# Kernel tuning notes

Hardware: AMD Instinct MI355X
Metric: run time of the kernel (lower is better)

Reference implementation:

```python
import jax, jax.numpy as jnp
import numpy as np

N_NODES = 50000
N_EDGES = 200000
IN_DIM = 16
NODE_DIM = 64
EDGE_DIM = 16
HIDDEN = 256
NUM_LAYERS = 4  # 1 NNConv + 3 GINConv


def setup_inputs() -> dict:
    key = jax.random.key(0)
    ks = jax.random.split(key, 20)
    s = 0.05
    inp = {
        "x": jax.random.normal(ks[0], (N_NODES, IN_DIM), dtype=jnp.float32),
        "edge_index": jax.random.randint(ks[1], (2, N_EDGES), 0, N_NODES, dtype=jnp.int64),
        "edge_attr": jax.random.normal(ks[2], (N_EDGES, EDGE_DIM), dtype=jnp.float32),
        # edge-NN (per-edge weight generator): attr_dim -> 256 -> 1024 -> in*out, ELU after each
        "enn_w1": jax.random.normal(ks[3], (EDGE_DIM, 256), dtype=jnp.float32) * s,
        "enn_b1": jnp.zeros((256,), dtype=jnp.float32),
        "enn_w2": jax.random.normal(ks[4], (256, 1024), dtype=jnp.float32) * s,
        "enn_b2": jnp.zeros((1024,), dtype=jnp.float32),
        "enn_w3": jax.random.normal(ks[5], (1024, IN_DIM * NODE_DIM), dtype=jnp.float32) * s,
        "enn_b3": jnp.zeros((IN_DIM * NODE_DIM,), dtype=jnp.float32),
        # NNConv root weight + bias
        "root_w": jax.random.normal(ks[6], (IN_DIM, NODE_DIM), dtype=jnp.float32) * s,
        "root_b": jnp.zeros((NODE_DIM,), dtype=jnp.float32),
        # 3 GIN MLPs (stacked): node_dim -> hidden -> hidden -> node_dim
        "gin_w1": jax.random.normal(ks[7], (3, NODE_DIM, HIDDEN), dtype=jnp.float32) * s,
        "gin_b1": jnp.zeros((3, HIDDEN), dtype=jnp.float32),
        "gin_w2": jax.random.normal(ks[8], (3, HIDDEN, HIDDEN), dtype=jnp.float32) * s,
        "gin_b2": jnp.zeros((3, HIDDEN), dtype=jnp.float32),
        "gin_w3": jax.random.normal(ks[9], (3, HIDDEN, NODE_DIM), dtype=jnp.float32) * s,
        "gin_b3": jnp.zeros((3, NODE_DIM), dtype=jnp.float32),
    }
    return inp


def _elu(x):
    return jax.nn.elu(x)


def reference(x, edge_index, edge_attr,
              enn_w1, enn_b1, enn_w2, enn_b2, enn_w3, enn_b3,
              root_w, root_b,
              gin_w1, gin_b1, gin_w2, gin_b2, gin_w3, gin_b3):
    src = edge_index[0]  # x_j (message source)
    dst = edge_index[1]  # i (aggregation target)

    # ---- Layer 0: NNConv with per-edge MLP-generated weights ----
    h = _elu(edge_attr @ enn_w1 + enn_b1)
    h = _elu(h @ enn_w2 + enn_b2)
    w_e = _elu(h @ enn_w3 + enn_b3).reshape(-1, IN_DIM, NODE_DIM)  # [E, in, out]
    msg = jnp.einsum('ei,eio->eo', x[src], w_e)                    # [E, node_dim]
    agg = jax.ops.segment_sum(msg, dst, num_segments=N_NODES)     # scatter-add
    x_cur = x @ root_w + agg + root_b                              # [N, node_dim]
    node_emb = [x_cur]

    # ---- Layers 1..3: GINConv (eps=0) with 3-layer MLP ----
    for l in range(NUM_LAYERS - 1):
        x_in = _elu(x_cur)
        nbr = jax.ops.segment_sum(x_in[src], dst, num_segments=N_NODES)
        h = x_in + nbr  # (1 + eps) * x + sum_j x_j, eps = 0
        h = _elu(h @ gin_w1[l] + gin_b1[l])
        h = _elu(h @ gin_w2[l] + gin_b2[l])
        x_cur = h @ gin_w3[l] + gin_b3[l]
        node_emb.append(x_cur)

    return jnp.stack(node_emb, axis=2)  # [N, node_dim, num_layers]
```

## Files before the change

kernel.cpp:

```cpp
#include <hip/hip_runtime.h>
#include <hip/hip_bf16.h>


#define NN 50000
#define EE 200000

typedef unsigned short u16;
typedef __attribute__((ext_vector_type(8))) short frag8;
typedef __attribute__((ext_vector_type(4))) float f32x4;

__device__ __forceinline__ float bf2f(u16 u) {
    union { unsigned int i; float f; } v; v.i = ((unsigned int)u) << 16; return v.f;
}
__device__ __forceinline__ u16 f2bf(float f) {
    union { float f; unsigned int i; } v; v.f = f;
    return (u16)((v.i + 0x7fffu + ((v.i >> 16) & 1u)) >> 16);
}
__device__ __forceinline__ float eluf(float v) {
    return v > 0.f ? v : __expf(v) - 1.f;
}

__global__ void probe_f32(const u16* __restrict__ raw, int* __restrict__ cnt) {
    int t = threadIdx.x;
    int c = 0;
    for (int j = t; j < 1024; j += 256) {
        unsigned e = (raw[j] >> 7) & 0xFF;
        if (e >= 0xBF) c++;
    }
    if (c) atomicAdd(cnt, c);
}
__global__ void cvt_bf16(const void* __restrict__ src, u16* __restrict__ dst, long n,
                         const int* __restrict__ cnt) {
    long i = (long)blockIdx.x * 256 + threadIdx.x;
    if (i >= n) return;
    if (*cnt >= 8) dst[i] = f2bf(((const float*)src)[i]);
    else           dst[i] = ((const u16*)src)[i];
}

__global__ void detect_idx64(const unsigned long long* __restrict__ p, int* __restrict__ flag) {
    long t = (long)blockIdx.x * 256 + threadIdx.x;
    if (t < EE) {
        unsigned long long v = p[t];
        if (v >> 31) atomicOr(flag, 1);
    }
}
__global__ void convert_idx(const void* __restrict__ raw, const int* __restrict__ flag,
                            int* __restrict__ s_out, int* __restrict__ d_out) {
    long t = (long)blockIdx.x * 256 + threadIdx.x;
    if (t >= EE) return;
    if (*flag) {
        const int* q = (const int*)raw;
        s_out[t] = q[t];
        d_out[t] = q[EE + t];
    } else {
        const long long* q = (const long long*)raw;
        s_out[t] = (int)q[t];
        d_out[t] = (int)q[EE + t];
    }
}

__global__ void transpose_bf16(const u16* __restrict__ in, u16* __restrict__ out, int K, int N) {
    long idx = (long)blockIdx.x * 256 + threadIdx.x;
    if (idx < (long)K * N) {
        int k = (int)(idx / N);
        int n = (int)(idx % N);
        out[(long)n * K + k] = in[idx];
    }
}

__global__ void edge_mlp1(const u16* __restrict__ attr, const u16* __restrict__ w1,
                          const u16* __restrict__ b1, u16* __restrict__ h1, int ce) {
    __shared__ u16 sa[256];
    const int t = threadIdx.x;
    const int e0 = blockIdx.x * 16;
    const int cnt = min(16, ce - e0);
    sa[t] = (t < cnt * 16) ? attr[(long)e0 * 16 + t] : (u16)0;
    float w[16];
    #pragma unroll
    for (int i = 0; i < 16; ++i) w[i] = bf2f(w1[i * 256 + t]);
    const float bb = bf2f(b1[t]);
    __syncthreads();
    for (int e = 0; e < cnt; ++e) {
        float v = bb;
        #pragma unroll
        for (int i = 0; i < 16; ++i) v += bf2f(sa[e * 16 + i]) * w[i];
        h1[(long)(e0 + e) * 256 + t] = f2bf(eluf(v));
    }
}

__device__ __forceinline__ void stage_tile(const u16* g, long row_base, long max_row,
                                           int kstride, int k0, u16* s, int t) {
    int wave = t >> 6;
    #pragma unroll
    for (int j = 0; j < 2; ++j) {
        int c = t + 256 * j;
        long r = row_base + (c >> 2);
        if (r > max_row) r = max_row;
        const u16* gp = g + r * (long)kstride + k0 + (c & 3) * 8;
        __builtin_amdgcn_global_load_lds(
            (__attribute__((address_space(1))) void*)(void*)gp,
            (__attribute__((address_space(3))) void*)((char*)s + wave * 1024 + j * 4096),
            16, 0, 0);
    }
}

__global__ __launch_bounds__(256)
void gemm_bt_bias_elu(const u16* __restrict__ A, const u16* __restrict__ BT,
                      const u16* __restrict__ bias, u16* __restrict__ C,
                      int M, int K, int N, int mpx, int lognt) {
    const int bid = blockIdx.x;
    const int xcd = bid & 7;
    const int j = bid >> 3;
    const int m_idx = xcd * mpx + (j >> lognt);
    const int n_idx = j & ((1 << lognt) - 1);
    const int num_m = (M + 127) >> 7;
    if (m_idx >= num_m) return;

    __shared__ __align__(16) u16 sA[128 * 32];
    __shared__ __align__(16) u16 sB[128 * 32];
    const int t = threadIdx.x;
    const int lane = t & 63;
    const int wave = t >> 6;
    const int wr = wave >> 1, wc = wave & 1;
    const int quad = lane >> 4, l16 = lane & 15;
    const long m0 = (long)m_idx * 128;
    const int n0 = n_idx * 128;

    f32x4 acc[4][4];
    const f32x4 z4 = {0.f, 0.f, 0.f, 0.f};
    #pragma unroll
    for (int mi = 0; mi < 4; ++mi)
        #pragma unroll
        for (int ni = 0; ni < 4; ++ni)
            acc[mi][ni] = z4;

    for (int k0 = 0; k0 < K; k0 += 32) {
        stage_tile(A, m0, (long)M - 1, K, k0, sA, t);
        stage_tile(BT, n0, (long)N - 1, K, k0, sB, t);
        __syncthreads();
        frag8 af[4], bfv[4];
        #pragma unroll
        for (int mi = 0; mi < 4; ++mi)
            af[mi] = *(const frag8*)(sA + (wr * 64 + mi * 16 + l16) * 32 + quad * 8);
        #pragma unroll
        for (int ni = 0; ni < 4; ++ni)
            bfv[ni] = *(const frag8*)(sB + (wc * 64 + ni * 16 + l16) * 32 + quad * 8);
        #pragma unroll
        for (int mi = 0; mi < 4; ++mi)
            #pragma unroll
            for (int ni = 0; ni < 4; ++ni)
                acc[mi][ni] = __builtin_amdgcn_mfma_f32_16x16x32_bf16(af[mi], bfv[ni], acc[mi][ni], 0, 0, 0);
        __syncthreads();
    }

    #pragma unroll
    for (int mi = 0; mi < 4; ++mi) {
        #pragma unroll
        for (int r = 0; r < 4; ++r) {
            long row = m0 + wr * 64 + mi * 16 + quad * 4 + r;
            if (row < M) {
                #pragma unroll
                for (int ni = 0; ni < 4; ++ni) {
                    int col = n0 + wc * 64 + ni * 16 + l16;
                    float v = acc[mi][ni][r] + bf2f(bias[col]);
                    C[row * (long)N + col] = f2bf(eluf(v));
                }
            }
        }
    }
}


#define QPHASE(PA0, PA1, PB0, PB1, QM, QN, LDA, LDB, VMW, STREG, SG, SRB, SRM, SCL, SKT) \
  do {                                                                           \
    if (LDA) {                                                                   \
      _Pragma("unroll")                                                          \
      for (int mi = 0; mi < 4; ++mi) {                                           \
        av[mi][0] = *(const frag8*)((PA0) + ((QM) * 4 + mi) * 2048);             \
        av[mi][1] = *(const frag8*)((PA1) + ((QM) * 4 + mi) * 2048);             \
      }                                                                          \
    }                                                                            \
    if ((LDB) >= 0) {                                                            \
      _Pragma("unroll")                                                          \
      for (int ni = 0; ni < 2; ++ni) {                                           \
        bv[(LDB) & 1][ni][0] = *(const frag8*)((PB0) + (((LDB) & 1) * 2 + ni) * 2048); \
        bv[(LDB) & 1][ni][1] = *(const frag8*)((PB1) + (((LDB) & 1) * 2 + ni) * 2048); \
      }                                                                          \
    }                                                                            \
    stage((STREG), (SG), (SRB), (SRM), (SKT), (SCL));                            \
    if (VMW) asm volatile("s_waitcnt vmcnt(4)" ::: "memory");                    \
    __builtin_amdgcn_s_barrier();                                                \
    __builtin_amdgcn_s_setprio(1);                                               \
    _Pragma("unroll")                                                            \
    for (int kk = 0; kk < 2; ++kk) {                                             \
      _Pragma("unroll")                                                          \
      for (int mi = 0; mi < 4; ++mi) {                                           \
        _Pragma("unroll")                                                        \
        for (int ni = 0; ni < 2; ++ni) {                                         \
          acc[(QM) * 4 + mi][(QN) * 2 + ni] =                                    \
              __builtin_amdgcn_mfma_f32_16x16x32_bf16(                           \
                  av[mi][kk], bv[(QN)][ni][kk],                                  \
                  acc[(QM) * 4 + mi][(QN) * 2 + ni], 0, 0, 0);                   \
        }                                                                        \
      }                                                                          \
    }                                                                            \
    __builtin_amdgcn_s_setprio(0);                                               \
    __builtin_amdgcn_s_barrier();                                                \
  } while (0)

__global__ __launch_bounds__(512, 2)
void gemm256p(const u16* __restrict__ A, const u16* __restrict__ BT,
              const u16* __restrict__ bias, u16* __restrict__ C,
              int M, int K, int N, int mpx, int lognt) {
    const int bid = blockIdx.x;
    const int xcd = bid & 7;
    const int j = bid >> 3;
    const int m_idx = xcd * mpx + (j >> lognt);
    const int n_idx = j & ((1 << lognt) - 1);
    const int num_m = (M + 255) >> 8;
    if (m_idx >= num_m) return;

    __shared__ __align__(16) u16 lds[2][4][8192];
    const int t = threadIdx.x;
    const int lane = t & 63;
    const int wave = t >> 6;
    const int wm = wave >> 2;
    const int wn = wave & 3;
    const int quad = lane >> 4, l16 = lane & 15;
    const long m0 = (long)m_idx * 256;
    const long n0 = (long)n_idx * 256;

    const int aoff0 = l16 * 128 + ((quad ^ (l16 & 3)) << 4) + (((l16 >> 2) & 1) << 6);
    const int aoff1 = aoff0 ^ 64;
    const int bex = (wn & 1) * 8192;
    const char* pAX0 = (const char*)&lds[0][wm][0] + aoff0;
    const char* pAX1 = (const char*)&lds[0][wm][0] + aoff1;
    const char* pAY0 = (const char*)&lds[1][wm][0] + aoff0;
    const char* pAY1 = (const char*)&lds[1][wm][0] + aoff1;
    const char* pBX0 = (const char*)&lds[0][2 + (wn >> 1)][0] + aoff0 + bex;
    const char* pBX1 = (const char*)&lds[0][2 + (wn >> 1)][0] + aoff1 + bex;
    const char* pBY0 = (const char*)&lds[1][2 + (wn >> 1)][0] + aoff0 + bex;
    const char* pBY1 = (const char*)&lds[1][2 + (wn >> 1)][0] + aoff1 + bex;

    const int gslot = (((lane & 7) ^ ((lane >> 3) & 7)) << 3);
    const int lane_row = lane >> 3;
    const long lane_go = (long)lane_row * K + gslot;

    auto stage = [&](u16* sreg, const u16* G, long rbase, long rmax, int kt, bool cl) {
        #pragma unroll
        for (int jj = 0; jj < 2; ++jj) {
            const int ck = wave * 2 + jj;
            const u16* gp;
            if (!cl) {
                gp = G + (rbase + ck * 8) * (long)K + ((long)kt << 6) + lane_go;
            } else {
                long r = rbase + ck * 8 + lane_row;
                if (r > rmax) r = rmax;
                gp = G + r * (long)K + ((long)kt << 6) + gslot;
            }
            __builtin_amdgcn_global_load_lds(
                (__attribute__((address_space(1))) void*)(void*)gp,
                (__attribute__((address_space(3))) void*)((char*)sreg + ck * 1024),
                16, 0, 0);
        }
    };

    f32x4 acc[8][4];
    const f32x4 z4 = {0.f, 0.f, 0.f, 0.f};
    #pragma unroll
    for (int mi = 0; mi < 8; ++mi)
        #pragma unroll
        for (int ni = 0; ni < 4; ++ni)
            acc[mi][ni] = z4;
    frag8 av[4][2];
    frag8 bv[2][2][2];

    const int ntk = K >> 6;
    const int niter = ntk >> 1;
    const long MM = (long)M - 1, NMX = (long)N - 1;
    const bool aclamp = (m0 + 255) > MM;

    stage(&lds[0][2][0], BT, n0,       NMX, 0, false);
    stage(&lds[0][3][0], BT, n0 + 128, NMX, 0, false);
    stage(&lds[0][0][0], A,  m0,       MM,  0, aclamp);
    stage(&lds[0][1][0], A,  m0 + 128, MM,  0, aclamp);
    stage(&lds[1][2][0], BT, n0,       NMX, 1, false);
    stage(&lds[1][3][0], BT, n0 + 128, NMX, 1, false);
    asm volatile("s_waitcnt vmcnt(4)" ::: "memory");
    __builtin_amdgcn_s_barrier();

    for (int it = 0; it < niter; ++it) {
        const int t1k = 2 * it + 1;
        int t2k = 2 * it + 2; if (t2k > ntk - 1) t2k = ntk - 1;
        int t3k = 2 * it + 3; if (t3k > ntk - 1) t3k = ntk - 1;

        QPHASE(pAX0, pAX1, pBX0, pBX1, 0, 0, 1,  0, 0, &lds[1][0][0], A,  m0,       MM,  aclamp, t1k);
        QPHASE(pAX0, pAX1, pBX0, pBX1, 0, 1, 0,  1, 0, &lds[1][1][0], A,  m0 + 128, MM,  aclamp, t1k);
        QPHASE(pAX0, pAX1, pBX0, pBX1, 1, 0, 1, -1, 0, &lds[0][2][0], BT, n0,       NMX, false,  t2k);
        QPHASE(pAX0, pAX1, pBX0, pBX1, 1, 1, 0, -1, 1, &lds[0][3][0], BT, n0 + 128, NMX, false,  t2k);
        QPHASE(pAY0, pAY1, pBY0, pBY1, 0, 0, 1,  0, 0, &lds[0][0][0], A,  m0,       MM,  aclamp, t2k);
        QPHASE(pAY0, pAY1, pBY0, pBY1, 0, 1, 0,  1, 0, &lds[0][1][0], A,  m0 + 128, MM,  aclamp, t2k);
        QPHASE(pAY0, pAY1, pBY0, pBY1, 1, 0, 1, -1, 0, &lds[1][2][0], BT, n0,       NMX, false,  t3k);
        QPHASE(pAY0, pAY1, pBY0, pBY1, 1, 1, 0, -1, 1, &lds[1][3][0], BT, n0 + 128, NMX, false,  t3k);
    }
    asm volatile("s_waitcnt vmcnt(0)" ::: "memory");

    #pragma unroll
    for (int mi = 0; mi < 8; ++mi) {
        #pragma unroll
        for (int r = 0; r < 4; ++r) {
            long row = m0 + wm * 128 + mi * 16 + quad * 4 + r;
            if (row < M) {
                #pragma unroll
                for (int ni = 0; ni < 4; ++ni) {
                    long col = n0 + wn * 64 + ni * 16 + l16;
                    float v = acc[mi][ni][r] + bf2f(bias[col]);
                    C[row * (long)N + col] = f2bf(eluf(v));
                }
            }
        }
    }
}

__global__ __launch_bounds__(256)
void gemm_bt_f32(const u16* __restrict__ A, const u16* __restrict__ BT,
                 const u16* __restrict__ bias, float* __restrict__ C,
                 int M, int K) {
    __shared__ __align__(16) u16 sA[256 * 32];
    __shared__ __align__(16) u16 sB[64 * 32];
    const int t = threadIdx.x;
    const int lane = t & 63;
    const int wave = t >> 6;
    const int quad = lane >> 4, l16 = lane & 15;
    const long m0 = (long)blockIdx.x * 256;

    f32x4 acc[4][4];
    const f32x4 z4 = {0.f, 0.f, 0.f, 0.f};
    #pragma unroll
    for (int mi = 0; mi < 4; ++mi)
        #pragma unroll
        for (int ni = 0; ni < 4; ++ni)
            acc[mi][ni] = z4;

    for (int k0 = 0; k0 < K; k0 += 32) {
        #pragma unroll
        for (int j = 0; j < 4; ++j) {
            int c = t + 256 * j;
            long r = m0 + (c >> 2);
            if (r > (long)M - 1) r = (long)M - 1;
            const u16* gp = A + r * (long)K + k0 + (c & 3) * 8;
            __builtin_amdgcn_global_load_lds(
                (__attribute__((address_space(1))) void*)(void*)gp,
                (__attribute__((address_space(3))) void*)((char*)sA + wave * 1024 + j * 4096),
                16, 0, 0);
        }
        {
            int c = t;
            const u16* gp = BT + (long)(c >> 2) * K + k0 + (c & 3) * 8;
            __builtin_amdgcn_global_load_lds(
                (__attribute__((address_space(1))) void*)(void*)gp,
                (__attribute__((address_space(3))) void*)((char*)sB + wave * 1024),
                16, 0, 0);
        }
        __syncthreads();
        frag8 af[4], bfv[4];
        #pragma unroll
        for (int mi = 0; mi < 4; ++mi)
            af[mi] = *(const frag8*)(sA + (wave * 64 + mi * 16 + l16) * 32 + quad * 8);
        #pragma unroll
        for (int ni = 0; ni < 4; ++ni)
            bfv[ni] = *(const frag8*)(sB + (ni * 16 + l16) * 32 + quad * 8);
        #pragma unroll
        for (int mi = 0; mi < 4; ++mi)
            #pragma unroll
            for (int ni = 0; ni < 4; ++ni)
                acc[mi][ni] = __builtin_amdgcn_mfma_f32_16x16x32_bf16(af[mi], bfv[ni], acc[mi][ni], 0, 0, 0);
        __syncthreads();
    }

    #pragma unroll
    for (int mi = 0; mi < 4; ++mi) {
        #pragma unroll
        for (int r = 0; r < 4; ++r) {
            long row = m0 + wave * 64 + mi * 16 + quad * 4 + r;
            if (row < M) {
                #pragma unroll
                for (int ni = 0; ni < 4; ++ni) {
                    int col = ni * 16 + l16;
                    C[row * 64 + col] = acc[mi][ni][r] + bf2f(bias[col]);
                }
            }
        }
    }
}

__global__ void nnconv_msg(const u16* __restrict__ we, const u16* __restrict__ x,
                           const int* __restrict__ src, const int* __restrict__ dst,
                           float* __restrict__ agg, int ce) {
    long idx = (long)blockIdx.x * 256 + threadIdx.x;
    if (idx >= (long)ce * 64) return;
    int o = (int)(idx & 63);
    long e = idx >> 6;
    const u16* wr = we + e * 1024;
    const u16* xr = x + (long)src[e] * 16;
    float v = 0.f;
    #pragma unroll
    for (int i = 0; i < 16; ++i)
        v += bf2f(xr[i]) * bf2f(wr[i * 64 + o]);
    atomicAdd(&agg[(long)dst[e] * 64 + o], v);
}

__global__ void add_root(const u16* __restrict__ x, const u16* __restrict__ rw,
                         const u16* __restrict__ rb, float* __restrict__ xcur) {
    long idx = (long)blockIdx.x * 256 + threadIdx.x;
    if (idx >= (long)NN * 64) return;
    int d = (int)(idx & 63);
    long n = idx >> 6;
    float v = bf2f(rb[d]);
    #pragma unroll
    for (int i = 0; i < 16; ++i)
        v += bf2f(x[n * 16 + i]) * bf2f(rw[i * 64 + d]);
    xcur[idx] += v;
}

__global__ void elu_bf16(const float* __restrict__ in, u16* __restrict__ o, long n) {
    long idx = (long)blockIdx.x * 256 + threadIdx.x;
    if (idx < n) o[idx] = f2bf(eluf(in[idx]));
}

__global__ void gin_scatter(const u16* __restrict__ xin, const int* __restrict__ src,
                            const int* __restrict__ dst, float* __restrict__ nbr) {
    long idx = (long)blockIdx.x * 256 + threadIdx.x;
    if (idx >= (long)EE * 64) return;
    int d = (int)(idx & 63);
    long e = idx >> 6;
    atomicAdd(&nbr[(long)dst[e] * 64 + d], bf2f(xin[(long)src[e] * 64 + d]));
}

__global__ void gin_combine(const u16* __restrict__ xin, const float* __restrict__ nbr,
                            u16* __restrict__ hin, long n) {
    long idx = (long)blockIdx.x * 256 + threadIdx.x;
    if (idx < n) hin[idx] = f2bf(bf2f(xin[idx]) + nbr[idx]);
}

__global__ void write_out(const float* __restrict__ e0, const float* __restrict__ e1,
                          const float* __restrict__ e2, const float* __restrict__ e3,
                          float* __restrict__ out) {
    long idx = (long)blockIdx.x * 256 + threadIdx.x;
    if (idx >= (long)NN * 64) return;
    float4 v = {e0[idx], e1[idx], e2[idx], e3[idx]};
    *(float4*)(out + idx * 4) = v;
}

extern "C" void kernel_launch(void* const* d_in, const int* in_sizes, int n_in,
                              void* d_out, int out_size, void* d_ws, size_t ws_size,
                              hipStream_t stream) {
    (void)in_sizes; (void)n_in; (void)out_size;
    const void* eidx = d_in[1];
    float* out = (float*)d_out;

    char* ws = (char*)d_ws;
    size_t off = 0;
    auto alloc = [&](size_t bytes) {
        char* p = ws + off;
        off += (bytes + 255) & ~(size_t)255;
        return p;
    };
    int* src32 = (int*)alloc((size_t)EE * 4);
    int* dst32 = (int*)alloc((size_t)EE * 4);
    int* flag  = (int*)alloc(256);
    int* cnt   = (int*)alloc(256);
    const int cv_idx[16] = {0, 2, 3, 4, 5, 6, 7, 8, 9, 10, 11, 12, 13, 14, 15, 16};
    const long cv_n[16]  = {800000, 3200000, 4096, 256, 262144, 1024, 1048576, 1024,
                            1024, 64, 49152, 768, 196608, 768, 49152, 192};
    u16* cv[16];
    for (int i = 0; i < 16; ++i) cv[i] = (u16*)alloc((size_t)cv_n[i] * 2);
    u16 *xc = cv[0], *eac = cv[1], *w1c = cv[2], *b1c = cv[3], *w2c = cv[4], *b2c = cv[5],
        *w3c = cv[6], *b3c = cv[7], *rwc = cv[8], *rbc = cv[9],
        *g1c = cv[10], *gb1c = cv[11], *g2c = cv[12], *gb2c = cv[13], *g3c = cv[14], *gb3c = cv[15];
    u16* w2t = (u16*)alloc((size_t)1024 * 256 * 2);
    u16* w3t = (u16*)alloc((size_t)1024 * 1024 * 2);
    u16* g1t = (u16*)alloc((size_t)3 * 256 * 64 * 2);
    u16* g2t = (u16*)alloc((size_t)3 * 256 * 256 * 2);
    u16* g3t = (u16*)alloc((size_t)3 * 64 * 256 * 2);
    float* emb[4];
    for (int l = 0; l < 4; ++l) emb[l] = (float*)alloc((size_t)NN * 64 * 4);
    float* agg = emb[0];
    char* scratch = (char*)alloc(0);
    size_t avail = (ws_size > off + 4096) ? (ws_size - off - 4096) : 0;

    long CE = (long)(avail / 4608) & ~127L;
    if (CE < 128) CE = 128;
    if (CE > 200064) CE = 200064;
    u16* h1c = (u16*)scratch;
    u16* h2c = (u16*)(scratch + (size_t)CE * 512);
    u16* wec = (u16*)(scratch + (size_t)CE * 2560);

    long gin_fixed = (long)NN * 64 * 4 + (long)NN * 64 * 2;
    long gin_avail = (long)avail - gin_fixed;
    if (gin_avail < 0) gin_avail = 0;
    long CN = (gin_avail / 1152) & ~255L;
    if (CN < 256) CN = 256;
    if (CN > 50176) CN = 50176;
    float* nbr = (float*)scratch;
    u16* xin   = (u16*)(scratch + (size_t)NN * 64 * 4);
    u16* hin   = (u16*)(scratch + gin_fixed);
    u16* hg1   = hin + (size_t)CN * 64;
    u16* hg2   = hg1 + (size_t)CN * 256;

    auto cdiv = [](long a, long b) { return (unsigned)((a + b - 1) / b); };

    hipMemsetAsync(cnt, 0, 4, stream);
    probe_f32<<<1, 256, 0, stream>>>((const u16*)d_in[0], cnt);
    for (int i = 0; i < 16; ++i)
        cvt_bf16<<<cdiv(cv_n[i], 256), 256, 0, stream>>>(d_in[cv_idx[i]], cv[i], cv_n[i], cnt);

    hipMemsetAsync(flag, 0, 4, stream);
    detect_idx64<<<cdiv(EE, 256), 256, 0, stream>>>((const unsigned long long*)eidx, flag);
    convert_idx<<<cdiv(EE, 256), 256, 0, stream>>>(eidx, flag, src32, dst32);

    transpose_bf16<<<cdiv(256 * 1024, 256), 256, 0, stream>>>(w2c, w2t, 256, 1024);
    transpose_bf16<<<cdiv(1024 * 1024, 256), 256, 0, stream>>>(w3c, w3t, 1024, 1024);
    for (int l = 0; l < 3; ++l) {
        transpose_bf16<<<cdiv(64 * 256, 256), 256, 0, stream>>>(g1c + l * 64 * 256, g1t + l * 256 * 64, 64, 256);
        transpose_bf16<<<cdiv(256 * 256, 256), 256, 0, stream>>>(g2c + l * 256 * 256, g2t + l * 256 * 256, 256, 256);
        transpose_bf16<<<cdiv(256 * 64, 256), 256, 0, stream>>>(g3c + l * 256 * 64, g3t + l * 64 * 256, 256, 64);
    }

    hipMemsetAsync(agg, 0, (size_t)NN * 64 * 4, stream);
    for (long e0 = 0; e0 < EE; e0 += CE) {
        int ce = (int)((EE - e0 < CE) ? (EE - e0) : CE);
        int mpx2 = cdiv(cdiv(ce, 256), 8);
        edge_mlp1<<<cdiv(ce, 16), 256, 0, stream>>>(eac + e0 * 16, w1c, b1c, h1c, ce);
        gemm256p<<<8 * mpx2 * 4, 512, 0, stream>>>(h1c, w2t, b2c, h2c, ce, 256, 1024, mpx2, 2);
        gemm256p<<<8 * mpx2 * 4, 512, 0, stream>>>(h2c, w3t, b3c, wec, ce, 1024, 1024, mpx2, 2);
        nnconv_msg<<<cdiv((long)ce * 64, 256), 256, 0, stream>>>(wec, xc, src32 + e0, dst32 + e0, agg, ce);
    }
    add_root<<<cdiv((long)NN * 64, 256), 256, 0, stream>>>(xc, rwc, rbc, agg);

    for (int l = 0; l < 3; ++l) {
        elu_bf16<<<cdiv((long)NN * 64, 256), 256, 0, stream>>>(emb[l], xin, (long)NN * 64);
        hipMemsetAsync(nbr, 0, (size_t)NN * 64 * 4, stream);
        gin_scatter<<<cdiv((long)EE * 64, 256), 256, 0, stream>>>(xin, src32, dst32, nbr);
        for (long n0 = 0; n0 < NN; n0 += CN) {
            int cn = (int)((NN - n0 < CN) ? (NN - n0) : CN);
            int mpx = cdiv(cdiv(cn, 128), 8);
            int mpx2 = cdiv(cdiv(cn, 256), 8);
            gin_combine<<<cdiv((long)cn * 64, 256), 256, 0, stream>>>(xin + n0 * 64, nbr + n0 * 64, hin, (long)cn * 64);
            gemm_bt_bias_elu<<<8 * mpx * 2, 256, 0, stream>>>(hin, g1t + l * 256 * 64, gb1c + l * 256, hg1, cn, 64, 256, mpx, 1);
            gemm256p<<<8 * mpx2 * 1, 512, 0, stream>>>(hg1, g2t + l * 256 * 256, gb2c + l * 256, hg2, cn, 256, 256, mpx2, 0);
            gemm_bt_f32<<<cdiv(cn, 256), 256, 0, stream>>>(hg2, g3t + l * 64 * 256, gb3c + l * 64, emb[l + 1] + n0 * 64, cn, 256);
        }
    }
    write_out<<<cdiv((long)NN * 64, 256), 256, 0, stream>>>(emb[0], emb[1], emb[2], emb[3], out);
}
```

Measured before the change: 1.538 ms.

## Fuse NNConv message into edge GEMM epilogue and batch small setup kernels

The last edge-MLP GEMM now applies bias and ELU to its accumulators, contracts them with the gathered source features in LDS, and atomically adds the result into the aggregate. This removes the materialised per-edge weight tensor and the separate message kernel. The 16 conversion launches and 11 transpose launches are each merged into a single kernel, and the GIN buffer memset is folded into the ELU kernel. The fused epilogue serialises the four column waves with barriers and issues more float atomics per edge, since each of four N-tiles adds partial sums.

```diff
diff --git a/kernel.cpp b/kernel.cpp
--- a/kernel.cpp
+++ b/kernel.cpp
@@ -29,12 +29,23 @@
     }
     if (c) atomicAdd(cnt, c);
 }
-__global__ void cvt_bf16(const void* __restrict__ src, u16* __restrict__ dst, long n,
-                         const int* __restrict__ cnt) {
-    long i = (long)blockIdx.x * 256 + threadIdx.x;
-    if (i >= n) return;
-    if (*cnt >= 8) dst[i] = f2bf(((const float*)src)[i]);
-    else           dst[i] = ((const u16*)src)[i];
+
+struct CvtPtrs { const void* src[16]; u16* dst[16]; };
+__global__ void cvt_all(CvtPtrs p, const int* __restrict__ cnt) {
+    constexpr long L[16] = {800000, 3200000, 4096, 256, 262144, 1024, 1048576, 1024,
+                            1024, 64, 49152, 768, 196608, 768, 49152, 192};
+    long idx = (long)blockIdx.x * 256 + threadIdx.x;
+    const bool isf32 = (*cnt >= 8);
+    long base = 0;
+    #pragma unroll
+    for (int i = 0; i < 16; ++i) {
+        if (idx >= base && idx < base + L[i]) {
+            long k = idx - base;
+            p.dst[i][k] = isf32 ? f2bf(((const float*)p.src[i])[k])
+                                : ((const u16*)p.src[i])[k];
+        }
+        base += L[i];
+    }
 }
 
 __global__ void detect_idx64(const unsigned long long* __restrict__ p, int* __restrict__ flag) {
@@ -59,12 +70,22 @@
     }
 }
 
-__global__ void transpose_bf16(const u16* __restrict__ in, u16* __restrict__ out, int K, int N) {
+struct TransPtrs { const u16* in[11]; u16* out[11]; };
+__global__ void transpose_all(TransPtrs p) {
+    constexpr int TK[11] = {256, 1024, 64, 256, 256, 64, 256, 256, 64, 256, 256};
+    constexpr int TN[11] = {1024, 1024, 256, 256, 64, 256, 256, 64, 256, 256, 64};
     long idx = (long)blockIdx.x * 256 + threadIdx.x;
-    if (idx < (long)K * N) {
-        int k = (int)(idx / N);
-        int n = (int)(idx % N);
-        out[(long)n * K + k] = in[idx];
+    long base = 0;
+    #pragma unroll
+    for (int i = 0; i < 11; ++i) {
+        const long sz = (long)TK[i] * TN[i];
+        if (idx >= base && idx < base + sz) {
+            long v = idx - base;
+            int k = (int)(v / TN[i]);
+            int n = (int)(v % TN[i]);
+            p.out[i][(long)n * TK[i] + k] = p.in[i][v];
+        }
+        base += sz;
     }
 }
 
@@ -208,6 +229,84 @@
     __builtin_amdgcn_s_barrier();                                                \
   } while (0)
 
+#define GEMM256_CORE()                                                                     \
+    __shared__ __align__(16) u16 lds[2][4][8192];                                          \
+    const int t = threadIdx.x;                                                             \
+    const int lane = t & 63;                                                               \
+    const int wave = t >> 6;                                                               \
+    const int wm = wave >> 2;                                                              \
+    const int wn = wave & 3;                                                               \
+    const int quad = lane >> 4, l16 = lane & 15;                                           \
+    const long m0 = (long)m_idx * 256;                                                     \
+    const long n0 = (long)n_idx * 256;                                                     \
+    const int aoff0 = l16 * 128 + ((quad ^ (l16 & 3)) << 4) + (((l16 >> 2) & 1) << 6);     \
+    const int aoff1 = aoff0 ^ 64;                                                          \
+    const int bex = (wn & 1) * 8192;                                                       \
+    const char* pAX0 = (const char*)&lds[0][wm][0] + aoff0;                                \
+    const char* pAX1 = (const char*)&lds[0][wm][0] + aoff1;                                \
+    const char* pAY0 = (const char*)&lds[1][wm][0] + aoff0;                                \
+    const char* pAY1 = (const char*)&lds[1][wm][0] + aoff1;                                \
+    const char* pBX0 = (const char*)&lds[0][2 + (wn >> 1)][0] + aoff0 + bex;               \
+    const char* pBX1 = (const char*)&lds[0][2 + (wn >> 1)][0] + aoff1 + bex;               \
+    const char* pBY0 = (const char*)&lds[1][2 + (wn >> 1)][0] + aoff0 + bex;               \
+    const char* pBY1 = (const char*)&lds[1][2 + (wn >> 1)][0] + aoff1 + bex;               \
+    const int gslot = (((lane & 7) ^ ((lane >> 3) & 7)) << 3);                             \
+    const int lane_row = lane >> 3;                                                        \
+    const long lane_go = (long)lane_row * K + gslot;                                       \
+    auto stage = [&](u16* sreg, const u16* G, long rbase, long rmax, int kt, bool cl) {    \
+        _Pragma("unroll")                                                                  \
+        for (int jj = 0; jj < 2; ++jj) {                                                   \
+            const int ck = wave * 2 + jj;                                                  \
+            const u16* gp;                                                                 \
+            if (!cl) {                                                                     \
+                gp = G + (rbase + ck * 8) * (long)K + ((long)kt << 6) + lane_go;           \
+            } else {                                                                       \
+                long r = rbase + ck * 8 + lane_row;                                        \
+                if (r > rmax) r = rmax;                                                    \
+                gp = G + r * (long)K + ((long)kt << 6) + gslot;                            \
+            }                                                                              \
+            __builtin_amdgcn_global_load_lds(                                              \
+                (__attribute__((address_space(1))) void*)(void*)gp,                        \
+                (__attribute__((address_space(3))) void*)((char*)sreg + ck * 1024),        \
+                16, 0, 0);                                                                 \
+        }                                                                                  \
+    };                                                                                     \
+    f32x4 acc[8][4];                                                                       \
+    const f32x4 z4 = {0.f, 0.f, 0.f, 0.f};                                                 \
+    _Pragma("unroll")                                                                      \
+    for (int mi = 0; mi < 8; ++mi)                                                         \
+        _Pragma("unroll")                                                                  \
+        for (int ni = 0; ni < 4; ++ni)                                                     \
+            acc[mi][ni] = z4;                                                              \
+    frag8 av[4][2];                                                                        \
+    frag8 bv[2][2][2];                                                                     \
+    const int ntk = K >> 6;                                                                \
+    const int niter = ntk >> 1;                                                            \
+    const long MM = (long)M - 1, NMX = (long)N - 1;                                        \
+    const bool aclamp = (m0 + 255) > MM;                                                   \
+    stage(&lds[0][2][0], BT, n0,       NMX, 0, false);                                     \
+    stage(&lds[0][3][0], BT, n0 + 128, NMX, 0, false);                                     \
+    stage(&lds[0][0][0], A,  m0,       MM,  0, aclamp);                                    \
+    stage(&lds[0][1][0], A,  m0 + 128, MM,  0, aclamp);                                    \
+    stage(&lds[1][2][0], BT, n0,       NMX, 1, false);                                     \
+    stage(&lds[1][3][0], BT, n0 + 128, NMX, 1, false);                                     \
+    asm volatile("s_waitcnt vmcnt(4)" ::: "memory");                                       \
+    __builtin_amdgcn_s_barrier();                                                          \
+    for (int it = 0; it < niter; ++it) {                                                   \
+        const int t1k = 2 * it + 1;                                                        \
+        int t2k = 2 * it + 2; if (t2k > ntk - 1) t2k = ntk - 1;                            \
+        int t3k = 2 * it + 3; if (t3k > ntk - 1) t3k = ntk - 1;                            \
+        QPHASE(pAX0, pAX1, pBX0, pBX1, 0, 0, 1,  0, 0, &lds[1][0][0], A,  m0,       MM,  aclamp, t1k); \
+        QPHASE(pAX0, pAX1, pBX0, pBX1, 0, 1, 0,  1, 0, &lds[1][1][0], A,  m0 + 128, MM,  aclamp, t1k); \
+        QPHASE(pAX0, pAX1, pBX0, pBX1, 1, 0, 1, -1, 0, &lds[0][2][0], BT, n0,       NMX, false,  t2k); \
+        QPHASE(pAX0, pAX1, pBX0, pBX1, 1, 1, 0, -1, 1, &lds[0][3][0], BT, n0 + 128, NMX, false,  t2k); \
+        QPHASE(pAY0, pAY1, pBY0, pBY1, 0, 0, 1,  0, 0, &lds[0][0][0], A,  m0,       MM,  aclamp, t2k); \
+        QPHASE(pAY0, pAY1, pBY0, pBY1, 0, 1, 0,  1, 0, &lds[0][1][0], A,  m0 + 128, MM,  aclamp, t2k); \
+        QPHASE(pAY0, pAY1, pBY0, pBY1, 1, 0, 1, -1, 0, &lds[1][2][0], BT, n0,       NMX, false,  t3k); \
+        QPHASE(pAY0, pAY1, pBY0, pBY1, 1, 1, 0, -1, 1, &lds[1][3][0], BT, n0 + 128, NMX, false,  t3k); \
+    }                                                                                      \
+    asm volatile("s_waitcnt vmcnt(0)" ::: "memory");
+
 __global__ __launch_bounds__(512, 2)
 void gemm256p(const u16* __restrict__ A, const u16* __restrict__ BT,
               const u16* __restrict__ bias, u16* __restrict__ C,
@@ -220,90 +319,7 @@
     const int num_m = (M + 255) >> 8;
     if (m_idx >= num_m) return;
 
-    __shared__ __align__(16) u16 lds[2][4][8192];
-    const int t = threadIdx.x;
-    const int lane = t & 63;
-    const int wave = t >> 6;
-    const int wm = wave >> 2;
-    const int wn = wave & 3;
-    const int quad = lane >> 4, l16 = lane & 15;
-    const long m0 = (long)m_idx * 256;
-    const long n0 = (long)n_idx * 256;
-
-    const int aoff0 = l16 * 128 + ((quad ^ (l16 & 3)) << 4) + (((l16 >> 2) & 1) << 6);
-    const int aoff1 = aoff0 ^ 64;
-    const int bex = (wn & 1) * 8192;
-    const char* pAX0 = (const char*)&lds[0][wm][0] + aoff0;
-    const char* pAX1 = (const char*)&lds[0][wm][0] + aoff1;
-    const char* pAY0 = (const char*)&lds[1][wm][0] + aoff0;
-    const char* pAY1 = (const char*)&lds[1][wm][0] + aoff1;
-    const char* pBX0 = (const char*)&lds[0][2 + (wn >> 1)][0] + aoff0 + bex;
-    const char* pBX1 = (const char*)&lds[0][2 + (wn >> 1)][0] + aoff1 + bex;
-    const char* pBY0 = (const char*)&lds[1][2 + (wn >> 1)][0] + aoff0 + bex;
-    const char* pBY1 = (const char*)&lds[1][2 + (wn >> 1)][0] + aoff1 + bex;
-
-    const int gslot = (((lane & 7) ^ ((lane >> 3) & 7)) << 3);
-    const int lane_row = lane >> 3;
-    const long lane_go = (long)lane_row * K + gslot;
-
-    auto stage = [&](u16* sreg, const u16* G, long rbase, long rmax, int kt, bool cl) {
-        #pragma unroll
-        for (int jj = 0; jj < 2; ++jj) {
-            const int ck = wave * 2 + jj;
-            const u16* gp;
-            if (!cl) {
-                gp = G + (rbase + ck * 8) * (long)K + ((long)kt << 6) + lane_go;
-            } else {
-                long r = rbase + ck * 8 + lane_row;
-                if (r > rmax) r = rmax;
-                gp = G + r * (long)K + ((long)kt << 6) + gslot;
-            }
-            __builtin_amdgcn_global_load_lds(
-                (__attribute__((address_space(1))) void*)(void*)gp,
-                (__attribute__((address_space(3))) void*)((char*)sreg + ck * 1024),
-                16, 0, 0);
-        }
-    };
-
-    f32x4 acc[8][4];
-    const f32x4 z4 = {0.f, 0.f, 0.f, 0.f};
-    #pragma unroll
-    for (int mi = 0; mi < 8; ++mi)
-        #pragma unroll
-        for (int ni = 0; ni < 4; ++ni)
-            acc[mi][ni] = z4;
-    frag8 av[4][2];
-    frag8 bv[2][2][2];
-
-    const int ntk = K >> 6;
-    const int niter = ntk >> 1;
-    const long MM = (long)M - 1, NMX = (long)N - 1;
-    const bool aclamp = (m0 + 255) > MM;
-
-    stage(&lds[0][2][0], BT, n0,       NMX, 0, false);
-    stage(&lds[0][3][0], BT, n0 + 128, NMX, 0, false);
-    stage(&lds[0][0][0], A,  m0,       MM,  0, aclamp);
-    stage(&lds[0][1][0], A,  m0 + 128, MM,  0, aclamp);
-    stage(&lds[1][2][0], BT, n0,       NMX, 1, false);
-    stage(&lds[1][3][0], BT, n0 + 128, NMX, 1, false);
-    asm volatile("s_waitcnt vmcnt(4)" ::: "memory");
-    __builtin_amdgcn_s_barrier();
-
-    for (int it = 0; it < niter; ++it) {
-        const int t1k = 2 * it + 1;
-        int t2k = 2 * it + 2; if (t2k > ntk - 1) t2k = ntk - 1;
-        int t3k = 2 * it + 3; if (t3k > ntk - 1) t3k = ntk - 1;
-
-        QPHASE(pAX0, pAX1, pBX0, pBX1, 0, 0, 1,  0, 0, &lds[1][0][0], A,  m0,       MM,  aclamp, t1k);
-        QPHASE(pAX0, pAX1, pBX0, pBX1, 0, 1, 0,  1, 0, &lds[1][1][0], A,  m0 + 128, MM,  aclamp, t1k);
-        QPHASE(pAX0, pAX1, pBX0, pBX1, 1, 0, 1, -1, 0, &lds[0][2][0], BT, n0,       NMX, false,  t2k);
-        QPHASE(pAX0, pAX1, pBX0, pBX1, 1, 1, 0, -1, 1, &lds[0][3][0], BT, n0 + 128, NMX, false,  t2k);
-        QPHASE(pAY0, pAY1, pBY0, pBY1, 0, 0, 1,  0, 0, &lds[0][0][0], A,  m0,       MM,  aclamp, t2k);
-        QPHASE(pAY0, pAY1, pBY0, pBY1, 0, 1, 0,  1, 0, &lds[0][1][0], A,  m0 + 128, MM,  aclamp, t2k);
-        QPHASE(pAY0, pAY1, pBY0, pBY1, 1, 0, 1, -1, 0, &lds[1][2][0], BT, n0,       NMX, false,  t3k);
-        QPHASE(pAY0, pAY1, pBY0, pBY1, 1, 1, 0, -1, 1, &lds[1][3][0], BT, n0 + 128, NMX, false,  t3k);
-    }
-    asm volatile("s_waitcnt vmcnt(0)" ::: "memory");
+    GEMM256_CORE()
 
     #pragma unroll
     for (int mi = 0; mi < 8; ++mi) {
@@ -319,6 +335,67 @@
                 }
             }
         }
+    }
+}
+
+__global__ __launch_bounds__(512, 2)
+void gemm256msg(const u16* __restrict__ A, const u16* __restrict__ BT,
+                const u16* __restrict__ bias,
+                const u16* __restrict__ xc, const int* __restrict__ srcp,
+                const int* __restrict__ dstp, float* __restrict__ agg,
+                int M, int K, int N, int mpx, int lognt) {
+    const int bid = blockIdx.x;
+    const int xcd = bid & 7;
+    const int j = bid >> 3;
+    const int m_idx = xcd * mpx + (j >> lognt);
+    const int n_idx = j & ((1 << lognt) - 1);
+    const int num_m = (M + 255) >> 8;
+    if (m_idx >= num_m) return;
+
+    GEMM256_CORE()
+
+    __syncthreads();
+    float* msgS = (float*)&lds[0][0][0];
+    float* sX   = (float*)((char*)&lds[0][0][0] + 65536);
+    int*   sDst = (int*)((char*)&lds[0][0][0] + 65536 + 4096);
+    const int ib4 = n_idx * 4;
+
+    for (int v = t; v < 16384; v += 512) msgS[v] = 0.f;
+    if (t < 256) {
+        long e = m0 + t;
+        long ec = (e <= MM) ? e : MM;
+        int s = srcp[ec];
+        sDst[t] = dstp[ec];
+        #pragma unroll
+        for (int jj = 0; jj < 4; ++jj)
+            sX[t * 4 + jj] = bf2f(xc[(long)s * 16 + ib4 + jj]);
+    }
+    __syncthreads();
+
+    for (int p = 0; p < 4; ++p) {
+        if (wn == p) {
+            #pragma unroll
+            for (int mi = 0; mi < 8; ++mi) {
+                #pragma unroll
+                for (int r = 0; r < 4; ++r) {
+                    int row = wm * 128 + mi * 16 + quad * 4 + r;
+                    float xv = sX[row * 4 + wn];
+                    #pragma unroll
+                    for (int ni = 0; ni < 4; ++ni) {
+                        int o = ni * 16 + l16;
+                        float we = eluf(acc[mi][ni][r] + bf2f(bias[n0 + wn * 64 + o]));
+                        msgS[row * 64 + o] += we * xv;
+                    }
+                }
+            }
+        }
+        __syncthreads();
+    }
+
+    for (int v = t; v < 16384; v += 512) {
+        int row = v >> 6, o = v & 63;
+        long e = m0 + row;
+        if (e < M) atomicAdd(&agg[(long)sDst[row] * 64 + o], msgS[v]);
     }
 }
 
@@ -394,22 +471,6 @@
     }
 }
 
-__global__ void nnconv_msg(const u16* __restrict__ we, const u16* __restrict__ x,
-                           const int* __restrict__ src, const int* __restrict__ dst,
-                           float* __restrict__ agg, int ce) {
-    long idx = (long)blockIdx.x * 256 + threadIdx.x;
-    if (idx >= (long)ce * 64) return;
-    int o = (int)(idx & 63);
-    long e = idx >> 6;
-    const u16* wr = we + e * 1024;
-    const u16* xr = x + (long)src[e] * 16;
-    float v = 0.f;
-    #pragma unroll
-    for (int i = 0; i < 16; ++i)
-        v += bf2f(xr[i]) * bf2f(wr[i * 64 + o]);
-    atomicAdd(&agg[(long)dst[e] * 64 + o], v);
-}
-
 __global__ void add_root(const u16* __restrict__ x, const u16* __restrict__ rw,
                          const u16* __restrict__ rb, float* __restrict__ xcur) {
     long idx = (long)blockIdx.x * 256 + threadIdx.x;
@@ -423,9 +484,10 @@
     xcur[idx] += v;
 }
 
-__global__ void elu_bf16(const float* __restrict__ in, u16* __restrict__ o, long n) {
+__global__ void elu_zero(const float* __restrict__ in, u16* __restrict__ o,
+                         float* __restrict__ nbr, long n) {
     long idx = (long)blockIdx.x * 256 + threadIdx.x;
-    if (idx < n) o[idx] = f2bf(eluf(in[idx]));
+    if (idx < n) { o[idx] = f2bf(eluf(in[idx])); nbr[idx] = 0.f; }
 }
 
 __global__ void gin_scatter(const u16* __restrict__ xin, const int* __restrict__ src,
@@ -489,12 +551,11 @@
     char* scratch = (char*)alloc(0);
     size_t avail = (ws_size > off + 4096) ? (ws_size - off - 4096) : 0;
 
-    long CE = (long)(avail / 4608) & ~127L;
-    if (CE < 128) CE = 128;
-    if (CE > 200064) CE = 200064;
+    long CE = (long)(avail / 2560) & ~255L;
+    if (CE < 256) CE = 256;
+    if (CE > 200192) CE = 200192;
     u16* h1c = (u16*)scratch;
     u16* h2c = (u16*)(scratch + (size_t)CE * 512);
-    u16* wec = (u16*)(scratch + (size_t)CE * 2560);
 
     long gin_fixed = (long)NN * 64 * 4 + (long)NN * 64 * 2;
     long gin_avail = (long)avail - gin_fixed;
@@ -512,19 +573,29 @@
 
     hipMemsetAsync(cnt, 0, 4, stream);
     probe_f32<<<1, 256, 0, stream>>>((const u16*)d_in[0], cnt);
-    for (int i = 0; i < 16; ++i)
-        cvt_bf16<<<cdiv(cv_n[i], 256), 256, 0, stream>>>(d_in[cv_idx[i]], cv[i], cv_n[i], cnt);
+    {
+        CvtPtrs cp;
+        for (int i = 0; i < 16; ++i) { cp.src[i] = d_in[cv_idx[i]]; cp.dst[i] = cv[i]; }
+        long total = 0;
+        for (int i = 0; i < 16; ++i) total += cv_n[i];
+        cvt_all<<<cdiv(total, 256), 256, 0, stream>>>(cp, cnt);
+    }
 
     hipMemsetAsync(flag, 0, 4, stream);
     detect_idx64<<<cdiv(EE, 256), 256, 0, stream>>>((const unsigned long long*)eidx, flag);
     convert_idx<<<cdiv(EE, 256), 256, 0, stream>>>(eidx, flag, src32, dst32);
 
-    transpose_bf16<<<cdiv(256 * 1024, 256), 256, 0, stream>>>(w2c, w2t, 256, 1024);
-    transpose_bf16<<<cdiv(1024 * 1024, 256), 256, 0, stream>>>(w3c, w3t, 1024, 1024);
-    for (int l = 0; l < 3; ++l) {
-        transpose_bf16<<<cdiv(64 * 256, 256), 256, 0, stream>>>(g1c + l * 64 * 256, g1t + l * 256 * 64, 64, 256);
-        transpose_bf16<<<cdiv(256 * 256, 256), 256, 0, stream>>>(g2c + l * 256 * 256, g2t + l * 256 * 256, 256, 256);
-        transpose_bf16<<<cdiv(256 * 64, 256), 256, 0, stream>>>(g3c + l * 256 * 64, g3t + l * 64 * 256, 256, 64);
+    {
+        TransPtrs tp;
+        tp.in[0] = w2c;  tp.out[0] = w2t;
+        tp.in[1] = w3c;  tp.out[1] = w3t;
+        for (int l = 0; l < 3; ++l) {
+            tp.in[2 + 3 * l] = g1c + l * 64 * 256;   tp.out[2 + 3 * l] = g1t + l * 256 * 64;
+            tp.in[3 + 3 * l] = g2c + l * 256 * 256;  tp.out[3 + 3 * l] = g2t + l * 256 * 256;
+            tp.in[4 + 3 * l] = g3c + l * 256 * 64;   tp.out[4 + 3 * l] = g3t + l * 64 * 256;
+        }
+        long total = 262144 + 1048576 + 3 * (16384 + 65536 + 16384);
+        transpose_all<<<cdiv(total, 256), 256, 0, stream>>>(tp);
     }
 
     hipMemsetAsync(agg, 0, (size_t)NN * 64 * 4, stream);
@@ -533,14 +604,13 @@
         int mpx2 = cdiv(cdiv(ce, 256), 8);
         edge_mlp1<<<cdiv(ce, 16), 256, 0, stream>>>(eac + e0 * 16, w1c, b1c, h1c, ce);
         gemm256p<<<8 * mpx2 * 4, 512, 0, stream>>>(h1c, w2t, b2c, h2c, ce, 256, 1024, mpx2, 2);
-        gemm256p<<<8 * mpx2 * 4, 512, 0, stream>>>(h2c, w3t, b3c, wec, ce, 1024, 1024, mpx2, 2);
-        nnconv_msg<<<cdiv((long)ce * 64, 256), 256, 0, stream>>>(wec, xc, src32 + e0, dst32 + e0, agg, ce);
+        gemm256msg<<<8 * mpx2 * 4, 512, 0, stream>>>(h2c, w3t, b3c, xc, src32 + e0, dst32 + e0,
+                                                     agg, ce, 1024, 1024, mpx2, 2);
     }
     add_root<<<cdiv((long)NN * 64, 256), 256, 0, stream>>>(xc, rwc, rbc, agg);
 
     for (int l = 0; l < 3; ++l) {
-        elu_bf16<<<cdiv((long)NN * 64, 256), 256, 0, stream>>>(emb[l], xin, (long)NN * 64);
-        hipMemsetAsync(nbr, 0, (size_t)NN * 64 * 4, stream);
+        elu_zero<<<cdiv((long)NN * 64, 256), 256, 0, stream>>>(emb[l], xin, nbr, (long)NN * 64);
         gin_scatter<<<cdiv((long)EE * 64, 256), 256, 0, stream>>>(xin, src32, dst32, nbr);
         for (long n0 = 0; n0 < NN; n0 += CN) {
             int cn = (int)((NN - n0 < CN) ? (NN - n0) : CN);
```

Result: slower. 1.589 ms (+3.4%).

## Batch conversion/transpose launches, use MFMA GEMM for edge layer 1, fuse zeroing

Applied to the files above, without the earlier changes.

Merges the 16 dtype-conversion launches and 11 transpose launches into single multi-segment kernels to cut launch overhead. Replaces the scalar edge_mlp1 kernel with the MFMA-based gemm_bt_bias_elu on zero-padded K=32 edge attributes and weights, and fuses the nbr memset into the ELU kernel. It also swaps the GIN hidden 256x256 GEMM from gemm256p to gemm_bt_bias_elu and rounds the edge chunk size to multiples of 256. The padding adds an extra EE*32 buffer and a pass over the edge attributes.

```diff
diff --git a/kernel.cpp b/kernel.cpp
--- a/kernel.cpp
+++ b/kernel.cpp
@@ -29,12 +29,23 @@
     }
     if (c) atomicAdd(cnt, c);
 }
-__global__ void cvt_bf16(const void* __restrict__ src, u16* __restrict__ dst, long n,
-                         const int* __restrict__ cnt) {
-    long i = (long)blockIdx.x * 256 + threadIdx.x;
-    if (i >= n) return;
-    if (*cnt >= 8) dst[i] = f2bf(((const float*)src)[i]);
-    else           dst[i] = ((const u16*)src)[i];
+
+struct CvtPtrs { const void* src[16]; u16* dst[16]; };
+__global__ void cvt_all(CvtPtrs p, const int* __restrict__ cnt) {
+    constexpr long L[16] = {800000, 3200000, 4096, 256, 262144, 1024, 1048576, 1024,
+                            1024, 64, 49152, 768, 196608, 768, 49152, 192};
+    long idx = (long)blockIdx.x * 256 + threadIdx.x;
+    const bool isf32 = (*cnt >= 8);
+    long base = 0;
+    #pragma unroll
+    for (int i = 0; i < 16; ++i) {
+        if (idx >= base && idx < base + L[i]) {
+            long k = idx - base;
+            p.dst[i][k] = isf32 ? f2bf(((const float*)p.src[i])[k])
+                                : ((const u16*)p.src[i])[k];
+        }
+        base += L[i];
+    }
 }
 
 __global__ void detect_idx64(const unsigned long long* __restrict__ p, int* __restrict__ flag) {
@@ -59,33 +70,37 @@
     }
 }
 
-__global__ void transpose_bf16(const u16* __restrict__ in, u16* __restrict__ out, int K, int N) {
-    long idx = (long)blockIdx.x * 256 + threadIdx.x;
-    if (idx < (long)K * N) {
-        int k = (int)(idx / N);
-        int n = (int)(idx % N);
-        out[(long)n * K + k] = in[idx];
-    }
-}
-
-__global__ void edge_mlp1(const u16* __restrict__ attr, const u16* __restrict__ w1,
-                          const u16* __restrict__ b1, u16* __restrict__ h1, int ce) {
-    __shared__ u16 sa[256];
-    const int t = threadIdx.x;
-    const int e0 = blockIdx.x * 16;
-    const int cnt = min(16, ce - e0);
-    sa[t] = (t < cnt * 16) ? attr[(long)e0 * 16 + t] : (u16)0;
-    float w[16];
-    #pragma unroll
-    for (int i = 0; i < 16; ++i) w[i] = bf2f(w1[i * 256 + t]);
-    const float bb = bf2f(b1[t]);
-    __syncthreads();
-    for (int e = 0; e < cnt; ++e) {
-        float v = bb;
-        #pragma unroll
-        for (int i = 0; i < 16; ++i) v += bf2f(sa[e * 16 + i]) * w[i];
-        h1[(long)(e0 + e) * 256 + t] = f2bf(eluf(v));
-    }
+struct TransPtrs { const u16* in[11]; u16* out[11]; };
+__global__ void transpose_all(TransPtrs p) {
+    constexpr int TK[11] = {256, 1024, 64, 256, 256, 64, 256, 256, 64, 256, 256};
+    constexpr int TN[11] = {1024, 1024, 256, 256, 64, 256, 256, 64, 256, 256, 64};
+    long idx = (long)blockIdx.x * 256 + threadIdx.x;
+    long base = 0;
+    #pragma unroll
+    for (int i = 0; i < 11; ++i) {
+        const long sz = (long)TK[i] * TN[i];
+        if (idx >= base && idx < base + sz) {
+            long v = idx - base;
+            int k = (int)(v / TN[i]);
+            int n = (int)(v % TN[i]);
+            p.out[i][(long)n * TK[i] + k] = p.in[i][v];
+        }
+        base += sz;
+    }
+}
+
+__global__ void pad_attr(const u16* __restrict__ a16, u16* __restrict__ a32) {
+    long idx = (long)blockIdx.x * 256 + threadIdx.x;
+    if (idx >= (long)EE * 32) return;
+    int k = (int)(idx & 31);
+    long e = idx >> 5;
+    a32[idx] = (k < 16) ? a16[e * 16 + k] : (u16)0;
+}
+__global__ void pad_w1t(const u16* __restrict__ w1, u16* __restrict__ w1t32) {
+    int idx = blockIdx.x * 256 + threadIdx.x;
+    if (idx >= 256 * 32) return;
+    int k = idx & 31, n = idx >> 5;
+    w1t32[idx] = (k < 16) ? w1[k * 256 + n] : (u16)0;
 }
 
 __device__ __forceinline__ void stage_tile(const u16* g, long row_base, long max_row,
@@ -423,9 +438,10 @@
     xcur[idx] += v;
 }
 
-__global__ void elu_bf16(const float* __restrict__ in, u16* __restrict__ o, long n) {
-    long idx = (long)blockIdx.x * 256 + threadIdx.x;
-    if (idx < n) o[idx] = f2bf(eluf(in[idx]));
+__global__ void elu_zero(const float* __restrict__ in, u16* __restrict__ o,
+                         float* __restrict__ nbr, long n) {
+    long idx = (long)blockIdx.x * 256 + threadIdx.x;
+    if (idx < n) { o[idx] = f2bf(eluf(in[idx])); nbr[idx] = 0.f; }
 }
 
 __global__ void gin_scatter(const u16* __restrict__ xin, const int* __restrict__ src,
@@ -483,15 +499,17 @@
     u16* g1t = (u16*)alloc((size_t)3 * 256 * 64 * 2);
     u16* g2t = (u16*)alloc((size_t)3 * 256 * 256 * 2);
     u16* g3t = (u16*)alloc((size_t)3 * 64 * 256 * 2);
+    u16* attr32 = (u16*)alloc((size_t)EE * 32 * 2);
+    u16* w1t32  = (u16*)alloc((size_t)256 * 32 * 2);
     float* emb[4];
     for (int l = 0; l < 4; ++l) emb[l] = (float*)alloc((size_t)NN * 64 * 4);
     float* agg = emb[0];
     char* scratch = (char*)alloc(0);
     size_t avail = (ws_size > off + 4096) ? (ws_size - off - 4096) : 0;
 
-    long CE = (long)(avail / 4608) & ~127L;
-    if (CE < 128) CE = 128;
-    if (CE > 200064) CE = 200064;
+    long CE = (long)(avail / 4608) & ~255L;
+    if (CE < 256) CE = 256;
+    if (CE > 200192) CE = 200192;
     u16* h1c = (u16*)scratch;
     u16* h2c = (u16*)(scratch + (size_t)CE * 512);
     u16* wec = (u16*)(scratch + (size_t)CE * 2560);
@@ -512,26 +530,39 @@
 
     hipMemsetAsync(cnt, 0, 4, stream);
     probe_f32<<<1, 256, 0, stream>>>((const u16*)d_in[0], cnt);
-    for (int i = 0; i < 16; ++i)
-        cvt_bf16<<<cdiv(cv_n[i], 256), 256, 0, stream>>>(d_in[cv_idx[i]], cv[i], cv_n[i], cnt);
+    {
+        CvtPtrs cp;
+        for (int i = 0; i < 16; ++i) { cp.src[i] = d_in[cv_idx[i]]; cp.dst[i] = cv[i]; }
+        long total = 0;
+        for (int i = 0; i < 16; ++i) total += cv_n[i];
+        cvt_all<<<cdiv(total, 256), 256, 0, stream>>>(cp, cnt);
+    }
 
     hipMemsetAsync(flag, 0, 4, stream);
     detect_idx64<<<cdiv(EE, 256), 256, 0, stream>>>((const unsigned long long*)eidx, flag);
     convert_idx<<<cdiv(EE, 256), 256, 0, stream>>>(eidx, flag, src32, dst32);
 
-    transpose_bf16<<<cdiv(256 * 1024, 256), 256, 0, stream>>>(w2c, w2t, 256, 1024);
-    transpose_bf16<<<cdiv(1024 * 1024, 256), 256, 0, stream>>>(w3c, w3t, 1024, 1024);
-    for (int l = 0; l < 3; ++l) {
-        transpose_bf16<<<cdiv(64 * 256, 256), 256, 0, stream>>>(g1c + l * 64 * 256, g1t + l * 256 * 64, 64, 256);
-        transpose_bf16<<<cdiv(256 * 256, 256), 256, 0, stream>>>(g2c + l * 256 * 256, g2t + l * 256 * 256, 256, 256);
-        transpose_bf16<<<cdiv(256 * 64, 256), 256, 0, stream>>>(g3c + l * 256 * 64, g3t + l * 64 * 256, 256, 64);
-    }
+    {
+        TransPtrs tp;
+        tp.in[0] = w2c;  tp.out[0] = w2t;
+        tp.in[1] = w3c;  tp.out[1] = w3t;
+        for (int l = 0; l < 3; ++l) {
+            tp.in[2 + 3 * l] = g1c + l * 64 * 256;   tp.out[2 + 3 * l] = g1t + l * 256 * 64;
+            tp.in[3 + 3 * l] = g2c + l * 256 * 256;  tp.out[3 + 3 * l] = g2t + l * 256 * 256;
+            tp.in[4 + 3 * l] = g3c + l * 256 * 64;   tp.out[4 + 3 * l] = g3t + l * 64 * 256;
+        }
+        long total = 262144 + 1048576 + 3 * (16384 + 65536 + 16384);
+        transpose_all<<<cdiv(total, 256), 256, 0, stream>>>(tp);
+    }
+    pad_attr<<<cdiv((long)EE * 32, 256), 256, 0, stream>>>(eac, attr32);
+    pad_w1t<<<cdiv(256 * 32, 256), 256, 0, stream>>>(w1c, w1t32);
 
     hipMemsetAsync(agg, 0, (size_t)NN * 64 * 4, stream);
     for (long e0 = 0; e0 < EE; e0 += CE) {
         int ce = (int)((EE - e0 < CE) ? (EE - e0) : CE);
+        int mpx  = cdiv(cdiv(ce, 128), 8);
         int mpx2 = cdiv(cdiv(ce, 256), 8);
-        edge_mlp1<<<cdiv(ce, 16), 256, 0, stream>>>(eac + e0 * 16, w1c, b1c, h1c, ce);
+        gemm_bt_bias_elu<<<8 * mpx * 2, 256, 0, stream>>>(attr32 + e0 * 32, w1t32, b1c, h1c, ce, 32, 256, mpx, 1);
         gemm256p<<<8 * mpx2 * 4, 512, 0, stream>>>(h1c, w2t, b2c, h2c, ce, 256, 1024, mpx2, 2);
         gemm256p<<<8 * mpx2 * 4, 512, 0, stream>>>(h2c, w3t, b3c, wec, ce, 1024, 1024, mpx2, 2);
         nnconv_msg<<<cdiv((long)ce * 64, 256), 256, 0, stream>>>(wec, xc, src32 + e0, dst32 + e0, agg, ce);
@@ -539,16 +570,14 @@
     add_root<<<cdiv((long)NN * 64, 256), 256, 0, stream>>>(xc, rwc, rbc, agg);
 
     for (int l = 0; l < 3; ++l) {
-        elu_bf16<<<cdiv((long)NN * 64, 256), 256, 0, stream>>>(emb[l], xin, (long)NN * 64);
-        hipMemsetAsync(nbr, 0, (size_t)NN * 64 * 4, stream);
+        elu_zero<<<cdiv((long)NN * 64, 256), 256, 0, stream>>>(emb[l], xin, nbr, (long)NN * 64);
         gin_scatter<<<cdiv((long)EE * 64, 256), 256, 0, stream>>>(xin, src32, dst32, nbr);
         for (long n0 = 0; n0 < NN; n0 += CN) {
             int cn = (int)((NN - n0 < CN) ? (NN - n0) : CN);
             int mpx = cdiv(cdiv(cn, 128), 8);
-            int mpx2 = cdiv(cdiv(cn, 256), 8);
             gin_combine<<<cdiv((long)cn * 64, 256), 256, 0, stream>>>(xin + n0 * 64, nbr + n0 * 64, hin, (long)cn * 64);
             gemm_bt_bias_elu<<<8 * mpx * 2, 256, 0, stream>>>(hin, g1t + l * 256 * 64, gb1c + l * 256, hg1, cn, 64, 256, mpx, 1);
-            gemm256p<<<8 * mpx2 * 1, 512, 0, stream>>>(hg1, g2t + l * 256 * 256, gb2c + l * 256, hg2, cn, 256, 256, mpx2, 0);
+            gemm_bt_bias_elu<<<8 * mpx * 2, 256, 0, stream>>>(hg1, g2t + l * 256 * 256, gb2c + l * 256, hg2, cn, 256, 256, mpx, 1);
             gemm_bt_f32<<<cdiv(cn, 256), 256, 0, stream>>>(hg2, g3t + l * 64 * 256, gb3c + l * 64, emb[l + 1] + n0 * 64, cn, 256);
         }
     }
```

After: 1.530 ms. About the same (-0.5%).
